# Kernel tuning notes

Measured on AMD Instinct MI355X. Metric: run time of the kernel, lower is better.

The kernel has to match this reference:

```python
import jax, jax.numpy as jnp
import numpy as np

DIM = 1024
B, S = 4, 2048

def setup_inputs() -> dict:
    key = jax.random.key(0)
    ks = jax.random.split(key, 4)
    x = jax.random.normal(ks[0], (B, S, DIM), dtype=jnp.float32)
    mask = jax.random.randint(ks[1], (B, S, S), 0, 2, dtype=jnp.int32)
    Wqkv = jax.random.normal(ks[2], (DIM, 3 * DIM), dtype=jnp.float32) / np.sqrt(DIM)
    bqkv = jnp.zeros((3 * DIM,), dtype=jnp.float32)
    Wout = jax.random.normal(ks[3], (DIM, DIM), dtype=jnp.float32) / np.sqrt(DIM)
    bout = jnp.zeros((DIM,), dtype=jnp.float32)
    return {"x": x, "mask": mask, "Wqkv": Wqkv, "bqkv": bqkv, "Wout": Wout, "bout": bout}

def reference(x, mask, Wqkv, bqkv, Wout, bout):
    dim = x.shape[-1]
    qkv = x @ Wqkv + bqkv                      # [B,S,3*dim]
    q, k, v = jnp.split(qkv, 3, axis=-1)       # each [B,S,dim]
    scores = jnp.einsum('bqd,bkd->bqk', q, k) / jnp.sqrt(jnp.float32(dim))
    # faithful to torch: masked positions set to 1e-10 (NOT -inf)
    scores = jnp.where(mask == 0, jnp.float32(1e-10), scores)
    attn = jax.nn.softmax(scores, axis=-1)     # dropout is identity in eval
    out = jnp.einsum('bqk,bkd->bqd', attn, v)  # [B,S,dim]
    return out @ Wout + bout
```

## Files before the change

### kernel.cpp

```cpp
#include <hip/hip_runtime.h>


typedef __attribute__((ext_vector_type(8))) short short8;
typedef __attribute__((ext_vector_type(4))) float f32x4;
typedef unsigned short u16;

#define SEQ 2048
#define NB 4

static __device__ __forceinline__ u16 f2bf(float f) {
    unsigned int u = __builtin_bit_cast(unsigned int, f);
    u += 0x7fffu + ((u >> 16) & 1u);
    return (u16)(u >> 16);
}
static __device__ __forceinline__ float bf2f(u16 h) {
    unsigned int u = ((unsigned int)h) << 16;
    return __builtin_bit_cast(float, u);
}

static __device__ __forceinline__ void gld16(const u16* l, const u16* g) {
    __builtin_amdgcn_global_load_lds(
        (__attribute__((address_space(1))) void*)(g),
        (__attribute__((address_space(3))) void*)(l),
        16, 0, 0);
}

__global__ __launch_bounds__(256) void cvt_bf16(const float* __restrict__ s,
                                                u16* __restrict__ d, long n) {
    long i = ((long)blockIdx.x * 256 + threadIdx.x) * 8;
    if (i >= n) return;
    f32x4 a = *(const f32x4*)(s + i);
    f32x4 b = *(const f32x4*)(s + i + 4);
    short8 o;
    o[0] = (short)f2bf(a.x); o[1] = (short)f2bf(a.y);
    o[2] = (short)f2bf(a.z); o[3] = (short)f2bf(a.w);
    o[4] = (short)f2bf(b.x); o[5] = (short)f2bf(b.y);
    o[6] = (short)f2bf(b.z); o[7] = (short)f2bf(b.w);
    *(short8*)(d + i) = o;
}

__global__ __launch_bounds__(256) void transpose_cvt(const float* __restrict__ in,
                                                     u16* __restrict__ out,
                                                     int R, int C) {
    __shared__ float t[32][33];
    const int c0 = blockIdx.x * 32;
    const int r0 = blockIdx.y * 32;
    const int x = threadIdx.x & 31;
    const int y = (threadIdx.x >> 5) * 4;
    #pragma unroll
    for (int i = 0; i < 4; i++)
        t[y + i][x] = in[(long)(r0 + y + i) * C + c0 + x];
    __syncthreads();
    #pragma unroll
    for (int i = 0; i < 4; i++)
        out[(long)(c0 + y + i) * R + r0 + x] = f2bf(t[x][y + i]);
}

__global__ __launch_bounds__(256) void transpose_v(const u16* __restrict__ qkv,
                                                   u16* __restrict__ vt) {
    __shared__ u16 t[32][33];
    const int b = blockIdx.z;
    const int s0 = blockIdx.y * 32;
    const int d0 = blockIdx.x * 32;
    const int x = threadIdx.x & 31;
    const int y = (threadIdx.x >> 5) * 4;
    const u16* src = qkv + (long)b * SEQ * 3072 + 2048;
    u16* dst = vt + (long)b * 1024 * SEQ;
    #pragma unroll
    for (int i = 0; i < 4; i++)
        t[y + i][x] = src[(long)(s0 + y + i) * 3072 + d0 + x];
    __syncthreads();
    #pragma unroll
    for (int i = 0; i < 4; i++)
        dst[(long)(d0 + y + i) * SEQ + s0 + x] = t[x][y + i];
}

template<int EPI>
__global__ __launch_bounds__(512) void gemm256d(
    const u16* __restrict__ Ap, long lda, long aBatch,
    const u16* __restrict__ Bp, long ldb, long bBatch,
    void* __restrict__ Cp, long ldc, long cBatch,
    const float* __restrict__ bias, float scale, int K, int nbx)
{
    __shared__ __attribute__((aligned(16))) u16 lds[2][4][8192];

    const int T = K >> 6;
    const int tid = threadIdx.x;
    const int lane = tid & 63;
    const int wave = tid >> 6;
    const int wm = wave >> 2;
    const int wn = wave & 3;
    const int m16 = lane & 15;
    const int quad = lane >> 4;
    const int b = blockIdx.z;

    const int nwg = gridDim.x;
    int wg = blockIdx.x;
    if ((nwg & 7) == 0)
        wg = (wg & 7) * (nwg >> 3) + (wg >> 3);
    const int bx = wg % nbx;
    const int by = wg / nbx;
    const long gm0 = (long)by * 256;
    const long gn0 = (long)bx * 256;

    const u16* A = Ap + (long)b * aBatch;
    const u16* B = Bp + (long)b * bBatch;

    const int rl = lane >> 3;
    const int lsl = ((lane & 7) ^ rl) * 8;
    const long aR = gm0 + wave * 8 + rl;
    const long bR = gn0 + (wave >> 2) * 64 + (wave & 3) * 8 + rl;

#define STGD(sl, tt) do { \
    const long kc_ = (long)(tt) << 6; \
    u16* l_ = &lds[sl][0][0]; \
    gld16(l_ + 0 * 8192 + wave * 512,       A + (aR)       * lda + kc_ + lsl); \
    gld16(l_ + 0 * 8192 + (8 + wave) * 512, A + (aR + 128) * lda + kc_ + lsl); \
    gld16(l_ + 1 * 8192 + wave * 512,       A + (aR + 64)  * lda + kc_ + lsl); \
    gld16(l_ + 1 * 8192 + (8 + wave) * 512, A + (aR + 192) * lda + kc_ + lsl); \
    gld16(l_ + 2 * 8192 + wave * 512,       B + (bR)       * ldb + kc_ + lsl); \
    gld16(l_ + 2 * 8192 + (8 + wave) * 512, B + (bR + 128) * ldb + kc_ + lsl); \
    gld16(l_ + 3 * 8192 + wave * 512,       B + (bR + 32)  * ldb + kc_ + lsl); \
    gld16(l_ + 3 * 8192 + (8 + wave) * 512, B + (bR + 160) * ldb + kc_ + lsl); \
} while (0)

    const int s0 = quad ^ (m16 & 7);
    const int aBase = (wm * 64 + m16) * 64;
    const int bBase = (wn * 32 + m16) * 64;
    const int aoff0 = aBase + s0 * 8, aoff1 = aBase + (s0 ^ 4) * 8;
    const int boff0 = bBase + s0 * 8, boff1 = bBase + (s0 ^ 4) * 8;

    short8 aF[4][2], b0F[2][2], b1F[2][2];
    f32x4 acc[8][4];
    #pragma unroll
    for (int mi = 0; mi < 8; mi++)
        #pragma unroll
        for (int ni = 0; ni < 4; ni++)
            acc[mi][ni] = (f32x4){0.f, 0.f, 0.f, 0.f};

#define TILE_COMPUTE(sl) do { \
    const u16* l = &lds[sl][0][0]; \
    _Pragma("unroll") \
    for (int mfl = 0; mfl < 4; ++mfl) { \
        aF[mfl][0] = *(const short8*)(l + aoff0 + mfl * 1024); \
        aF[mfl][1] = *(const short8*)(l + aoff1 + mfl * 1024); \
    } \
    _Pragma("unroll") \
    for (int nj = 0; nj < 2; ++nj) { \
        b0F[nj][0] = *(const short8*)(l + 2 * 8192 + boff0 + nj * 1024); \
        b0F[nj][1] = *(const short8*)(l + 2 * 8192 + boff1 + nj * 1024); \
        b1F[nj][0] = *(const short8*)(l + 3 * 8192 + boff0 + nj * 1024); \
        b1F[nj][1] = *(const short8*)(l + 3 * 8192 + boff1 + nj * 1024); \
    } \
    _Pragma("unroll") \
    for (int mi = 0; mi < 4; ++mi) \
        _Pragma("unroll") \
        for (int nj = 0; nj < 4; ++nj) { \
            const short8* bf = (nj < 2) ? &b0F[nj][0] : &b1F[nj - 2][0]; \
            acc[mi][nj] = __builtin_amdgcn_mfma_f32_16x16x32_bf16( \
                aF[mi][0], bf[0], acc[mi][nj], 0, 0, 0); \
            acc[mi][nj] = __builtin_amdgcn_mfma_f32_16x16x32_bf16( \
                aF[mi][1], bf[1], acc[mi][nj], 0, 0, 0); \
        } \
    _Pragma("unroll") \
    for (int mfl = 0; mfl < 4; ++mfl) { \
        aF[mfl][0] = *(const short8*)(l + 1 * 8192 + aoff0 + mfl * 1024); \
        aF[mfl][1] = *(const short8*)(l + 1 * 8192 + aoff1 + mfl * 1024); \
    } \
    _Pragma("unroll") \
    for (int mi = 0; mi < 4; ++mi) \
        _Pragma("unroll") \
        for (int nj = 0; nj < 4; ++nj) { \
            const short8* bf = (nj < 2) ? &b0F[nj][0] : &b1F[nj - 2][0]; \
            acc[4 + mi][nj] = __builtin_amdgcn_mfma_f32_16x16x32_bf16( \
                aF[mi][0], bf[0], acc[4 + mi][nj], 0, 0, 0); \
            acc[4 + mi][nj] = __builtin_amdgcn_mfma_f32_16x16x32_bf16( \
                aF[mi][1], bf[1], acc[4 + mi][nj], 0, 0, 0); \
        } \
} while (0)

    STGD(0, 0);
    __syncthreads();

    for (int t = 0; t < T; t += 2) {
        if (t + 1 < T) STGD(1, t + 1);
        TILE_COMPUTE(0);
        __syncthreads();
        if (t + 2 < T) STGD(0, t + 2);
        TILE_COMPUTE(1);
        __syncthreads();
    }

    const long row0 = gm0 + wm * 128 + quad * 4;
    const long colbase = gn0 + wn * 64 + m16;
    if (EPI == 0 || EPI == 1) {
        u16* C = (u16*)Cp + (long)b * cBatch;
        float bv[4];
        #pragma unroll
        for (int ni = 0; ni < 4; ++ni)
            bv[ni] = (EPI == 0 && bias)
                   ? bias[colbase + (ni >> 1) * 32 + (ni & 1) * 16] : 0.f;
        #pragma unroll
        for (int mi = 0; mi < 8; ++mi) {
            const long rb = row0 + (mi >> 2) * 64 + (mi & 3) * 16;
            #pragma unroll
            for (int r = 0; r < 4; ++r) {
                u16* Crow = C + (rb + r) * ldc + colbase;
                #pragma unroll
                for (int ni = 0; ni < 4; ++ni) {
                    const float vv = (EPI == 1) ? acc[mi][ni][r] * scale
                                                : acc[mi][ni][r] + bv[ni];
                    Crow[(ni >> 1) * 32 + (ni & 1) * 16] = f2bf(vv);
                }
            }
        }
    } else {
        float* C = (float*)Cp + (long)b * cBatch;
        float bv[4];
        #pragma unroll
        for (int ni = 0; ni < 4; ++ni)
            bv[ni] = bias ? bias[colbase + (ni >> 1) * 32 + (ni & 1) * 16] : 0.f;
        #pragma unroll
        for (int mi = 0; mi < 8; ++mi) {
            const long rb = row0 + (mi >> 2) * 64 + (mi & 3) * 16;
            #pragma unroll
            for (int r = 0; r < 4; ++r) {
                float* Crow = C + (rb + r) * ldc + colbase;
                #pragma unroll
                for (int ni = 0; ni < 4; ++ni)
                    Crow[(ni >> 1) * 32 + (ni & 1) * 16] = acc[mi][ni][r] + bv[ni];
            }
        }
    }
#undef STGD
#undef TILE_COMPUTE
}

template<int EPI>
__global__ __launch_bounds__(256) void gemm128(
    const u16* __restrict__ Ap, long lda, long aBatch,
    const u16* __restrict__ Bp, long ldb, long bBatch,
    void* __restrict__ Cp, long ldc, long cBatch,
    const float* __restrict__ bias,
    float scale, int K)
{
    __shared__ __attribute__((aligned(16))) u16 As[128 * 64];
    __shared__ __attribute__((aligned(16))) u16 Bs[128 * 64];

    const int tid = threadIdx.x;
    const int lane = tid & 63;
    const int wave = tid >> 6;
    const int b = blockIdx.z;
    const long m0 = (long)blockIdx.y * 128;
    const long n0 = (long)blockIdx.x * 128;

    const u16* A = Ap + (long)b * aBatch;
    const u16* B = Bp + (long)b * bBatch;

    const int wm = (wave >> 1) * 64;
    const int wn = (wave & 1) * 64;
    const int m16 = lane & 15;
    const int quad = lane >> 4;

    const int srow = lane >> 3;
    const int skk = (lane & 7) * 8;

    f32x4 acc[4][4];
    #pragma unroll
    for (int mi = 0; mi < 4; mi++)
        #pragma unroll
        for (int ni = 0; ni < 4; ni++)
            acc[mi][ni] = (f32x4){0.f, 0.f, 0.f, 0.f};

    for (int k0 = 0; k0 < K; k0 += 64) {
        #pragma unroll
        for (int c = 0; c < 4; c++) {
            const int r = wave * 32 + c * 8 + srow;
            gld16(As + (wave * 4 + c) * 512, A + (m0 + r) * lda + k0 + skk);
            gld16(Bs + (wave * 4 + c) * 512, B + (n0 + r) * ldb + k0 + skk);
        }
        __syncthreads();

        #pragma unroll
        for (int ks = 0; ks < 2; ks++) {
            short8 af[4], bf[4];
            #pragma unroll
            for (int i = 0; i < 4; i++) {
                af[i] = *(const short8*)&As[(wm + i * 16 + m16) * 64 + ks * 32 + quad * 8];
                bf[i] = *(const short8*)&Bs[(wn + i * 16 + m16) * 64 + ks * 32 + quad * 8];
            }
            #pragma unroll
            for (int mi = 0; mi < 4; mi++)
                #pragma unroll
                for (int ni = 0; ni < 4; ni++)
                    acc[mi][ni] = __builtin_amdgcn_mfma_f32_16x16x32_bf16(
                        af[mi], bf[ni], acc[mi][ni], 0, 0, 0);
        }
        __syncthreads();
    }

    const long row_base = m0 + wm + quad * 4;
    const long colbase = n0 + wn + m16;
    if (EPI == 0) {
        u16* C = (u16*)Cp + (long)b * cBatch;
        float bv[4];
        #pragma unroll
        for (int ni = 0; ni < 4; ni++)
            bv[ni] = bias ? bias[colbase + ni * 16] : 0.f;
        #pragma unroll
        for (int mi = 0; mi < 4; mi++)
            #pragma unroll
            for (int r = 0; r < 4; r++) {
                u16* Crow = C + (row_base + mi * 16 + r) * ldc + colbase;
                #pragma unroll
                for (int ni = 0; ni < 4; ni++)
                    Crow[ni * 16] = f2bf(acc[mi][ni][r] + bv[ni]);
            }
    } else if (EPI == 1) {
        u16* C = (u16*)Cp + (long)b * cBatch;
        #pragma unroll
        for (int mi = 0; mi < 4; mi++)
            #pragma unroll
            for (int r = 0; r < 4; r++) {
                u16* Crow = C + (row_base + mi * 16 + r) * ldc + colbase;
                #pragma unroll
                for (int ni = 0; ni < 4; ni++)
                    Crow[ni * 16] = f2bf(acc[mi][ni][r] * scale);
            }
    } else {
        float* C = (float*)Cp + (long)b * cBatch;
        float bv[4];
        #pragma unroll
        for (int ni = 0; ni < 4; ni++)
            bv[ni] = bias ? bias[colbase + ni * 16] : 0.f;
        #pragma unroll
        for (int mi = 0; mi < 4; mi++)
            #pragma unroll
            for (int r = 0; r < 4; r++) {
                float* Crow = C + (row_base + mi * 16 + r) * ldc + colbase;
                #pragma unroll
                for (int ni = 0; ni < 4; ni++)
                    Crow[ni * 16] = acc[mi][ni][r] + bv[ni];
            }
    }
}

__global__ __launch_bounds__(256) void softmax2048(u16* __restrict__ S,
                                                   const int* __restrict__ mask) {
    const long row = blockIdx.x;
    u16* p = S + row * SEQ;
    const int* mrow = mask + row * SEQ;
    const int tid = threadIdx.x;

    short8 v = *(const short8*)(p + tid * 8);
    uint4 mw0 = *(const uint4*)(mrow + tid * 8);
    uint4 mw1 = *(const uint4*)(mrow + tid * 8 + 4);
    const unsigned int* mwv = (const unsigned int*)&mw0;

    float f[8];
    #pragma unroll
    for (int j = 0; j < 8; j++) {
        const unsigned int mv = (j < 4) ? mwv[j] : ((const unsigned int*)&mw1)[j - 4];
        f[j] = (mv == 0u) ? 1e-10f : bf2f((u16)v[j]);
    }

    float m = f[0];
    #pragma unroll
    for (int j = 1; j < 8; j++) m = fmaxf(m, f[j]);
    #pragma unroll
    for (int i = 1; i < 64; i <<= 1) m = fmaxf(m, __shfl_xor(m, i));

    __shared__ float redm[4], reds[4];
    if ((tid & 63) == 0) redm[tid >> 6] = m;
    __syncthreads();
    m = fmaxf(fmaxf(redm[0], redm[1]), fmaxf(redm[2], redm[3]));

    float e[8], s = 0.f;
    #pragma unroll
    for (int j = 0; j < 8; j++) { e[j] = __expf(f[j] - m); s += e[j]; }
    #pragma unroll
    for (int i = 1; i < 64; i <<= 1) s += __shfl_xor(s, i);
    if ((tid & 63) == 0) reds[tid >> 6] = s;
    __syncthreads();
    s = reds[0] + reds[1] + reds[2] + reds[3];

    const float inv = 1.f / s;
    short8 o;
    #pragma unroll
    for (int j = 0; j < 8; j++) o[j] = (short)f2bf(e[j] * inv);
    *(short8*)(p + tid * 8) = o;
}

extern "C" void kernel_launch(void* const* d_in, const int* in_sizes, int n_in,
                              void* d_out, int out_size, void* d_ws, size_t ws_size,
                              hipStream_t stream) {
    const float* x    = (const float*)d_in[0];
    const int*   mask = (const int*)d_in[1];
    const float* Wqkv = (const float*)d_in[2];
    const float* bqkv = (const float*)d_in[3];
    const float* Wout = (const float*)d_in[4];
    const float* bout = (const float*)d_in[5];
    float* out = (float*)d_out;

    char* ws = (char*)d_ws;
    u16* xh   = (u16*)(ws + 0);
    u16* wqt  = (u16*)(ws + 16777216);
    u16* sc   = (u16*)(ws + 0);
    u16* wot  = (u16*)(ws + 33554432);
    u16* qkv  = (u16*)(ws + 35651584);
    u16* attn = (u16*)(ws + 35651584);
    u16* vt   = (u16*)(ws + 85983232);

    cvt_bf16<<<4096, 256, 0, stream>>>(x, xh, 8388608);
    transpose_cvt<<<dim3(96, 32), 256, 0, stream>>>(Wqkv, wqt, 1024, 3072);
    transpose_cvt<<<dim3(32, 32), 256, 0, stream>>>(Wout, wot, 1024, 1024);

    gemm256d<0><<<dim3(384, 1, 1), 512, 0, stream>>>(
        xh, 1024, 0, wqt, 1024, 0, qkv, 3072, 0, bqkv, 1.f, 1024, 12);

    transpose_v<<<dim3(32, 64, NB), 256, 0, stream>>>(qkv, vt);

    gemm256d<1><<<dim3(64, 1, NB), 512, 0, stream>>>(
        qkv, 3072, (long)SEQ * 3072, qkv + 1024, 3072, (long)SEQ * 3072,
        sc, SEQ, (long)SEQ * SEQ, nullptr, 0.03125f, 1024, 8);

    softmax2048<<<dim3(NB * SEQ), 256, 0, stream>>>(sc, mask);

    gemm128<0><<<dim3(8, 16, NB), 256, 0, stream>>>(
        sc, SEQ, (long)SEQ * SEQ, vt, SEQ, (long)1024 * SEQ,
        attn, 1024, (long)SEQ * 1024, nullptr, 1.f, 2048);

    gemm128<2><<<dim3(8, 64, 1), 256, 0, stream>>>(
        attn, 1024, 0, wot, 1024, 0, out, 1024, 0, bout, 1.f, 1024);
}
```

Measured before the change: 221.4 us.

## Double-buffer LDS with XOR swizzle and XCD-aware tile mapping in 128x128 GEMM

Rewrites the 128x128 GEMM used for attn@V and the output projection. LDS is double-buffered so the async global-to-LDS loads for the next K tile overlap MFMA work on the current one, halving the barriers per tile. Rows are stored with an XOR swizzle to avoid LDS bank conflicts on fragment reads. Workgroups use a 1D grid remapped so consecutive tiles land on the same XCD for L2 reuse. The cost is doubled LDS (64KB) per block and a launch bound that asks for 2 blocks per CU.

```diff
diff --git a/kernel.cpp b/kernel.cpp
--- a/kernel.cpp
+++ b/kernel.cpp
@@ -237,34 +237,57 @@
 }
 
 template<int EPI>
-__global__ __launch_bounds__(256) void gemm128(
+__global__ __launch_bounds__(256, 2) void gemm128d(
     const u16* __restrict__ Ap, long lda, long aBatch,
     const u16* __restrict__ Bp, long ldb, long bBatch,
     void* __restrict__ Cp, long ldc, long cBatch,
-    const float* __restrict__ bias,
-    float scale, int K)
+    const float* __restrict__ bias, float scale, int K, int nbx)
 {
-    __shared__ __attribute__((aligned(16))) u16 As[128 * 64];
-    __shared__ __attribute__((aligned(16))) u16 Bs[128 * 64];
-
+    __shared__ __attribute__((aligned(16))) u16 lds[2][2][8192];
+
+    const int T = K >> 6;
     const int tid = threadIdx.x;
     const int lane = tid & 63;
     const int wave = tid >> 6;
+    const int wm = wave >> 1;
+    const int wn = wave & 1;
+    const int m16 = lane & 15;
+    const int quad = lane >> 4;
     const int b = blockIdx.z;
-    const long m0 = (long)blockIdx.y * 128;
-    const long n0 = (long)blockIdx.x * 128;
+
+    const int nwg = gridDim.x;
+    int wg = blockIdx.x;
+    if ((nwg & 7) == 0)
+        wg = (wg & 7) * (nwg >> 3) + (wg >> 3);
+    const int bx = wg % nbx;
+    const int by = wg / nbx;
+    const long m0 = (long)by * 128;
+    const long n0 = (long)bx * 128;
 
     const u16* A = Ap + (long)b * aBatch;
     const u16* B = Bp + (long)b * bBatch;
 
-    const int wm = (wave >> 1) * 64;
-    const int wn = (wave & 1) * 64;
-    const int m16 = lane & 15;
-    const int quad = lane >> 4;
-
-    const int srow = lane >> 3;
-    const int skk = (lane & 7) * 8;
-
+    const int rl = lane >> 3;
+    const int lsl = ((lane & 7) ^ rl) * 8;
+    const long aR = m0 + wave * 8 + rl;
+    const long bR = n0 + wave * 8 + rl;
+
+#define STG128(sl, tt) do { \
+    const long kc_ = (long)(tt) << 6; \
+    _Pragma("unroll") \
+    for (int i_ = 0; i_ < 4; ++i_) { \
+        gld16(&lds[sl][0][(i_ * 4 + wave) * 512], A + (aR + i_ * 32) * lda + kc_ + lsl); \
+        gld16(&lds[sl][1][(i_ * 4 + wave) * 512], B + (bR + i_ * 32) * ldb + kc_ + lsl); \
+    } \
+} while (0)
+
+    const int s0 = quad ^ (m16 & 7);
+    const int aoff0 = (wm * 64 + m16) * 64 + s0 * 8;
+    const int aoff1 = (wm * 64 + m16) * 64 + (s0 ^ 4) * 8;
+    const int boff0 = (wn * 64 + m16) * 64 + s0 * 8;
+    const int boff1 = (wn * 64 + m16) * 64 + (s0 ^ 4) * 8;
+
+    short8 aF[4][2], bF[4][2];
     f32x4 acc[4][4];
     #pragma unroll
     for (int mi = 0; mi < 4; mi++)
@@ -272,77 +295,80 @@
         for (int ni = 0; ni < 4; ni++)
             acc[mi][ni] = (f32x4){0.f, 0.f, 0.f, 0.f};
 
-    for (int k0 = 0; k0 < K; k0 += 64) {
-        #pragma unroll
-        for (int c = 0; c < 4; c++) {
-            const int r = wave * 32 + c * 8 + srow;
-            gld16(As + (wave * 4 + c) * 512, A + (m0 + r) * lda + k0 + skk);
-            gld16(Bs + (wave * 4 + c) * 512, B + (n0 + r) * ldb + k0 + skk);
-        }
+#define TILE128(sl) do { \
+    const u16* la = &lds[sl][0][0]; \
+    const u16* lb = &lds[sl][1][0]; \
+    _Pragma("unroll") \
+    for (int mf = 0; mf < 4; ++mf) { \
+        aF[mf][0] = *(const short8*)(la + aoff0 + mf * 1024); \
+        aF[mf][1] = *(const short8*)(la + aoff1 + mf * 1024); \
+    } \
+    _Pragma("unroll") \
+    for (int nj = 0; nj < 4; ++nj) { \
+        bF[nj][0] = *(const short8*)(lb + boff0 + nj * 1024); \
+        bF[nj][1] = *(const short8*)(lb + boff1 + nj * 1024); \
+    } \
+    _Pragma("unroll") \
+    for (int mi = 0; mi < 4; ++mi) \
+        _Pragma("unroll") \
+        for (int nj = 0; nj < 4; ++nj) { \
+            acc[mi][nj] = __builtin_amdgcn_mfma_f32_16x16x32_bf16( \
+                aF[mi][0], bF[nj][0], acc[mi][nj], 0, 0, 0); \
+            acc[mi][nj] = __builtin_amdgcn_mfma_f32_16x16x32_bf16( \
+                aF[mi][1], bF[nj][1], acc[mi][nj], 0, 0, 0); \
+        } \
+} while (0)
+
+    STG128(0, 0);
+    __syncthreads();
+
+    for (int t = 0; t < T; t += 2) {
+        if (t + 1 < T) STG128(1, t + 1);
+        TILE128(0);
         __syncthreads();
-
-        #pragma unroll
-        for (int ks = 0; ks < 2; ks++) {
-            short8 af[4], bf[4];
-            #pragma unroll
-            for (int i = 0; i < 4; i++) {
-                af[i] = *(const short8*)&As[(wm + i * 16 + m16) * 64 + ks * 32 + quad * 8];
-                bf[i] = *(const short8*)&Bs[(wn + i * 16 + m16) * 64 + ks * 32 + quad * 8];
-            }
-            #pragma unroll
-            for (int mi = 0; mi < 4; mi++)
-                #pragma unroll
-                for (int ni = 0; ni < 4; ni++)
-                    acc[mi][ni] = __builtin_amdgcn_mfma_f32_16x16x32_bf16(
-                        af[mi], bf[ni], acc[mi][ni], 0, 0, 0);
-        }
+        if (t + 2 < T) STG128(0, t + 2);
+        TILE128(1);
         __syncthreads();
     }
 
-    const long row_base = m0 + wm + quad * 4;
-    const long colbase = n0 + wn + m16;
-    if (EPI == 0) {
+    const long row0 = m0 + wm * 64 + quad * 4;
+    const long colbase = n0 + wn * 64 + m16;
+    if (EPI == 0 || EPI == 1) {
         u16* C = (u16*)Cp + (long)b * cBatch;
         float bv[4];
         #pragma unroll
-        for (int ni = 0; ni < 4; ni++)
-            bv[ni] = bias ? bias[colbase + ni * 16] : 0.f;
-        #pragma unroll
-        for (int mi = 0; mi < 4; mi++)
+        for (int ni = 0; ni < 4; ++ni)
+            bv[ni] = (EPI == 0 && bias) ? bias[colbase + ni * 16] : 0.f;
+        #pragma unroll
+        for (int mi = 0; mi < 4; ++mi)
             #pragma unroll
-            for (int r = 0; r < 4; r++) {
-                u16* Crow = C + (row_base + mi * 16 + r) * ldc + colbase;
+            for (int r = 0; r < 4; ++r) {
+                u16* Crow = C + (row0 + mi * 16 + r) * ldc + colbase;
                 #pragma unroll
-                for (int ni = 0; ni < 4; ni++)
-                    Crow[ni * 16] = f2bf(acc[mi][ni][r] + bv[ni]);
-            }
-    } else if (EPI == 1) {
-        u16* C = (u16*)Cp + (long)b * cBatch;
-        #pragma unroll
-        for (int mi = 0; mi < 4; mi++)
-            #pragma unroll
-            for (int r = 0; r < 4; r++) {
-                u16* Crow = C + (row_base + mi * 16 + r) * ldc + colbase;
-                #pragma unroll
-                for (int ni = 0; ni < 4; ni++)
-                    Crow[ni * 16] = f2bf(acc[mi][ni][r] * scale);
+                for (int ni = 0; ni < 4; ++ni) {
+                    const float vv = (EPI == 1) ? acc[mi][ni][r] * scale
+                                                : acc[mi][ni][r] + bv[ni];
+                    Crow[ni * 16] = f2bf(vv);
+                }
             }
     } else {
         float* C = (float*)Cp + (long)b * cBatch;
         float bv[4];
         #pragma unroll
-        for (int ni = 0; ni < 4; ni++)
+        for (int ni = 0; ni < 4; ++ni)
             bv[ni] = bias ? bias[colbase + ni * 16] : 0.f;
         #pragma unroll
-        for (int mi = 0; mi < 4; mi++)
+        for (int mi = 0; mi < 4; ++mi)
             #pragma unroll
-            for (int r = 0; r < 4; r++) {
-                float* Crow = C + (row_base + mi * 16 + r) * ldc + colbase;
+            for (int r = 0; r < 4; ++r) {
+                float* Crow = C + (row0 + mi * 16 + r) * ldc + colbase;
                 #pragma unroll
-                for (int ni = 0; ni < 4; ni++)
+                for (int ni = 0; ni < 4; ++ni)
                     Crow[ni * 16] = acc[mi][ni][r] + bv[ni];
             }
     }
+#undef STG128
+#undef TILE128
 }
 
 __global__ __launch_bounds__(256) void softmax2048(u16* __restrict__ S,
@@ -426,10 +452,10 @@
 
     softmax2048<<<dim3(NB * SEQ), 256, 0, stream>>>(sc, mask);
 
-    gemm128<0><<<dim3(8, 16, NB), 256, 0, stream>>>(
+    gemm128d<0><<<dim3(128, 1, NB), 256, 0, stream>>>(
         sc, SEQ, (long)SEQ * SEQ, vt, SEQ, (long)1024 * SEQ,
-        attn, 1024, (long)SEQ * 1024, nullptr, 1.f, 2048);
-
-    gemm128<2><<<dim3(8, 64, 1), 256, 0, stream>>>(
-        attn, 1024, 0, wot, 1024, 0, out, 1024, 0, bout, 1.f, 1024);
-}
+        attn, 1024, (long)SEQ * 1024, nullptr, 1.f, 2048, 8);
+
+    gemm128d<2><<<dim3(512, 1, 1), 256, 0, stream>>>(
+        attn, 1024, 0, wot, 1024, 0, out, 1024, 0, bout, 1.f, 1024, 8);
+}
```

New measurement: 198.4 us. 1.12x faster.
